# Performance work log

Hardware: AMD Instinct MI355X
Metric: run time of the kernel (lower is better)

The kernel has to match this reference:

```python
import jax, jax.numpy as jnp
import numpy as np

B, T, C = 4, 2048, 1024
WIN = 16


def setup_inputs() -> dict:
    key = jax.random.key(0)
    ks = jax.random.split(key, 5)
    s = 1.0 / np.sqrt(C)
    return {
        "x": jax.random.normal(ks[0], (B, T, C), dtype=jnp.float32),
        "Wq": jax.random.normal(ks[1], (C, C), dtype=jnp.float32) * s,
        "bq": jnp.zeros((C,), jnp.float32),
        "Wk": jax.random.normal(ks[2], (C, C), dtype=jnp.float32) * s,
        "bk": jnp.zeros((C,), jnp.float32),
        "Wv": jax.random.normal(ks[3], (C, C), dtype=jnp.float32) * s,
        "bv": jnp.zeros((C,), jnp.float32),
        "Wo": jax.random.normal(ks[4], (C, C), dtype=jnp.float32) * s,
        "bo": jnp.zeros((C,), jnp.float32),
        "window": WIN,
    }


def reference(x, Wq, bq, Wk, bk, Wv, bv, Wo, bo, window):
    Bn, Tn, Cn = x.shape
    half = window // 2
    W = 2 * half + 1  # keys per query (window [t-half, t+half])
    q = x @ Wq.T + bq
    k = x @ Wk.T + bk
    v = x @ Wv.T + bv
    offs = jnp.arange(-half, half + 1)              # [W]
    tpos = jnp.arange(Tn)                            # [T]
    idx = tpos[:, None] + offs[None, :]              # [T, W]
    valid = (idx >= 0) & (idx < Tn)                  # [T, W]
    idx_c = jnp.clip(idx, 0, Tn - 1)
    k_win = k[:, idx_c, :]                           # [B, T, W, C]
    v_win = v[:, idx_c, :]                           # [B, T, W, C]
    scale = 1.0 / jnp.sqrt(jnp.asarray(Cn, x.dtype))
    scores = jnp.einsum('btc,btwc->btw', q, k_win) * scale
    scores = jnp.where(valid[None, :, :], scores, jnp.finfo(x.dtype).min)
    attn = jax.nn.softmax(scores, axis=-1)           # [B, T, W]
    ctx = jnp.einsum('btw,btwc->btc', attn, v_win)   # [B, T, C]
    return ctx @ Wo.T + bo
```

## Files before the change

### kernel.cpp

```cpp
#include <hip/hip_runtime.h>
#include <cstdint>
#include <cstddef>

#define B_ 4
#define T_ 2048
#define C_ 1024
#define M_ (B_ * T_)
#define HALF_ 8
#define W_ 17
#define QKV_STRIDE 3072

typedef unsigned short u16;
typedef _Float16 half8 __attribute__((ext_vector_type(8)));
typedef _Float16 half2_t __attribute__((ext_vector_type(2)));
typedef float f32x16 __attribute__((ext_vector_type(16)));

__device__ __forceinline__ float dot16(half8 a, half8 b, float acc) {
#if __has_builtin(__builtin_amdgcn_fdot2)
    const half2_t* pa = (const half2_t*)&a;
    const half2_t* pb = (const half2_t*)&b;
#pragma unroll
    for (int e = 0; e < 4; ++e) acc = __builtin_amdgcn_fdot2(pa[e], pb[e], acc, false);
#else
#pragma unroll
    for (int e = 0; e < 8; ++e) acc += (float)a[e] * (float)b[e];
#endif
    return acc;
}

__device__ __forceinline__ ushort4 cvt4(float4 v) {
    ushort4 o;
    _Float16 a = (_Float16)v.x; o.x = __builtin_bit_cast(unsigned short, a);
    _Float16 b = (_Float16)v.y; o.y = __builtin_bit_cast(unsigned short, b);
    _Float16 c = (_Float16)v.z; o.z = __builtin_bit_cast(unsigned short, c);
    _Float16 d = (_Float16)v.w; o.w = __builtin_bit_cast(unsigned short, d);
    return o;
}


__global__ void prologue(const float* __restrict__ x,
                         const float* __restrict__ Wq, const float* __restrict__ Wk,
                         const float* __restrict__ Wv, const float* __restrict__ Wo,
                         const float* __restrict__ bq, const float* __restrict__ bk,
                         const float* __restrict__ bv,
                         u16* __restrict__ xf, u16* __restrict__ wfq,
                         u16* __restrict__ wfo, float* __restrict__ bcat) {
    const int blk = blockIdx.x;
    const int tid = threadIdx.x;
    if (blk < 4096) {
        const int wid  = blk * 4 + (tid >> 6);
        const int lane = tid & 63;
        const int mt = wid >> 6;
        const int ks = wid & 63;
        const int row = mt * 32 + (lane & 31);
        const int col = ks * 16 + (lane >> 5) * 8;
        const float4* s = (const float4*)(x + (size_t)row * C_ + col);
        ushort4* d = (ushort4*)(xf + (((size_t)mt * 64 + ks) * 64 + lane) * 8);
        d[0] = cvt4(s[0]);
        d[1] = cvt4(s[1]);
        return;
    }
    if (blk >= 6144) {
        int i = (blk - 6144) * 256 + tid;
        const float* src = (i < 1024) ? bq : (i < 2048) ? bk : bv;
        bcat[i] = src[i & 1023];
        return;
    }
    int c = (blk - 4096) * 256 + tid;
    const float* src;
    u16* dst;
    int cc;
    if (c < 393216) {
        int mat = c / 131072;
        src = (mat == 0) ? Wq : (mat == 1) ? Wk : Wv;
        dst = wfq;  cc = c;  c = c % 131072;
    } else {
        src = Wo;  dst = wfo;  cc = c - 393216;  c = cc;
    }
    const int nt_local = c >> 12;
    const int ks   = (c >> 6) & 63;
    const int lane = c & 63;
    const int row = nt_local * 32 + (lane & 31);
    const int col = ks * 16 + (lane >> 5) * 8;
    const float4* s = (const float4*)(src + (size_t)row * C_ + col);
    ushort4* d = (ushort4*)(dst + (size_t)cc * 8);
    d[0] = cvt4(s[0]);
    d[1] = cvt4(s[1]);
}

template <int OUT_F16>
__global__ __launch_bounds__(256) void gemm_frag(
    const u16* __restrict__ Afrag, const u16* __restrict__ Bfrag,
    const float* __restrict__ bias, void* __restrict__ Cout,
    int Ndim, int nks)
{
    const int tid  = threadIdx.x;
    const int lane = tid & 63;
    const int wave = tid >> 6;
    const int m0 = blockIdx.y * 128;
    const int wm = (wave >> 1) * 64;
    const int mt0 = blockIdx.y * 4 + (wave >> 1) * 2;
    const int wnt = blockIdx.x * 4 + (wave & 1) * 2;

    const u16* Af0 = Afrag + ((size_t)mt0 * nks) * 512 + lane * 8;
    const u16* Af1 = Af0 + (size_t)nks * 512;
    const u16* Bf0 = Bfrag + ((size_t)wnt * nks) * 512 + lane * 8;
    const u16* Bf1 = Bf0 + (size_t)nks * 512;

    f32x16 acc00, acc01, acc10, acc11;
#pragma unroll
    for (int r = 0; r < 16; ++r) { acc00[r] = 0.f; acc01[r] = 0.f; acc10[r] = 0.f; acc11[r] = 0.f; }

#pragma unroll 4
    for (int ks = 0; ks < nks; ++ks) {
        const size_t off = (size_t)ks * 512;
        half8 a0 = *(const half8*)(Af0 + off);
        half8 a1 = *(const half8*)(Af1 + off);
        half8 b0 = *(const half8*)(Bf0 + off);
        half8 b1 = *(const half8*)(Bf1 + off);
        acc00 = __builtin_amdgcn_mfma_f32_32x32x16_f16(a0, b0, acc00, 0, 0, 0);
        acc01 = __builtin_amdgcn_mfma_f32_32x32x16_f16(a0, b1, acc01, 0, 0, 0);
        acc10 = __builtin_amdgcn_mfma_f32_32x32x16_f16(a1, b0, acc10, 0, 0, 0);
        acc11 = __builtin_amdgcn_mfma_f32_32x32x16_f16(a1, b1, acc11, 0, 0, 0);
    }

    f32x16 accs[2][2] = {{acc00, acc01}, {acc10, acc11}};
#pragma unroll
    for (int i = 0; i < 2; ++i) {
#pragma unroll
        for (int j = 0; j < 2; ++j) {
            const int col = (wnt + j) * 32 + (lane & 31);
            const float bv = bias[col];
#pragma unroll
            for (int reg = 0; reg < 16; ++reg) {
                const int row = m0 + wm + i * 32 + (reg & 3) + 8 * (reg >> 2) + 4 * (lane >> 5);
                float val = accs[i][j][reg] + bv;
                if (OUT_F16) {
                    _Float16 h = (_Float16)val;
                    ((u16*)Cout)[(size_t)row * Ndim + col] = __builtin_bit_cast(unsigned short, h);
                } else {
                    ((float*)Cout)[(size_t)row * Ndim + col] = val;
                }
            }
        }
    }
}

__global__ __launch_bounds__(256) void attn_local(
    const u16* __restrict__ qkv, u16* __restrict__ ctxf)
{
    const int wid  = blockIdx.x * 4 + (threadIdx.x >> 6);
    const int lane = threadIdx.x & 63;
    const int b = wid >> 11;
    const int t = wid & (T_ - 1);
    const int base = b * T_;
    const size_t qrow = (size_t)(base + t) * QKV_STRIDE;
    const int c0 = lane * 8;

    half8 q0 = *(const half8*)(qkv + qrow + c0);
    half8 q1 = *(const half8*)(qkv + qrow + 512 + c0);

    float s[W_];
#pragma unroll
    for (int o = 0; o < W_; ++o) {
        int j = t - HALF_ + o;
        int jc = min(max(j, 0), T_ - 1);
        const size_t kb = (size_t)(base + jc) * QKV_STRIDE + 1024;
        half8 k0v = *(const half8*)(qkv + kb + c0);
        half8 k1v = *(const half8*)(qkv + kb + 512 + c0);
        float d = dot16(q1, k1v, dot16(q0, k0v, 0.f));
#pragma unroll
        for (int off = 32; off > 0; off >>= 1)
            d += __shfl_xor(d, off);
        s[o] = (j == jc) ? d * 0.03125f : -3.0e38f;
    }

    float mx = s[0];
#pragma unroll
    for (int o = 1; o < W_; ++o) mx = fmaxf(mx, s[o]);
    float den = 0.f;
#pragma unroll
    for (int o = 0; o < W_; ++o) den += __expf(s[o] - mx);
    const float inv = 1.f / den;

    float acc0[8], acc1[8];
#pragma unroll
    for (int e = 0; e < 8; ++e) { acc0[e] = 0.f; acc1[e] = 0.f; }
#pragma unroll
    for (int o = 0; o < W_; ++o) {
        int j = t - HALF_ + o;
        int jc = min(max(j, 0), T_ - 1);
        const float wt = __expf(s[o] - mx) * inv;
        const size_t vb_ = (size_t)(base + jc) * QKV_STRIDE + 2048;
        half8 v0 = *(const half8*)(qkv + vb_ + c0);
        half8 v1 = *(const half8*)(qkv + vb_ + 512 + c0);
#pragma unroll
        for (int e = 0; e < 8; ++e) {
            acc0[e] += wt * (float)v0[e];
            acc1[e] += wt * (float)v1[e];
        }
    }

    half8 o0, o1;
#pragma unroll
    for (int e = 0; e < 8; ++e) { o0[e] = (_Float16)acc0[e]; o1[e] = (_Float16)acc1[e]; }

    const int m = base + t;
    const int mt = m >> 5;
    const int rowin = (m & 31) + 32 * (lane & 1);
    const size_t ch0 = ((size_t)mt * 64 + (lane >> 1)) * 64 + rowin;
    const size_t ch1 = ((size_t)mt * 64 + 32 + (lane >> 1)) * 64 + rowin;
    *(half8*)(ctxf + ch0 * 8) = o0;
    *(half8*)(ctxf + ch1 * 8) = o1;
}

extern "C" void kernel_launch(void* const* d_in, const int* in_sizes, int n_in,
                              void* d_out, int out_size, void* d_ws, size_t ws_size,
                              hipStream_t stream) {
    const float* x  = (const float*)d_in[0];
    const float* Wq = (const float*)d_in[1];
    const float* bq = (const float*)d_in[2];
    const float* Wk = (const float*)d_in[3];
    const float* bk = (const float*)d_in[4];
    const float* Wv = (const float*)d_in[5];
    const float* bv = (const float*)d_in[6];
    const float* Wo = (const float*)d_in[7];
    const float* bo = (const float*)d_in[8];
    float* out = (float*)d_out;

    u16* xf   = (u16*)d_ws;
    u16* wfq  = xf   + (size_t)M_ * C_;
    u16* wfo  = wfq  + (size_t)3 * C_ * C_;
    u16* qkvh = wfo  + (size_t)C_ * C_;
    u16* ctxf = qkvh + (size_t)M_ * QKV_STRIDE;
    float* bcat = (float*)(ctxf + (size_t)M_ * C_);

    prologue<<<6156, 256, 0, stream>>>(x, Wq, Wk, Wv, Wo, bq, bk, bv,
                                       xf, wfq, wfo, bcat);

    dim3 gqkv(QKV_STRIDE / 128, M_ / 128);
    gemm_frag<1><<<gqkv, 256, 0, stream>>>(xf, wfq, bcat, qkvh, QKV_STRIDE, 64);

    attn_local<<<M_ / 4, 256, 0, stream>>>(qkvh, ctxf);

    dim3 go(C_ / 128, M_ / 128);
    gemm_frag<0><<<go, 256, 0, stream>>>(ctxf, wfo, bo, out, C_, 64);
}
```

Before: 228.0 us.

## Rewrite fragment GEMM with LDS triple-buffered async loads and 8-wave blocks

Replaces the direct-from-global fragment GEMM with a 512-thread, 256x128-tile kernel that stages A and B fragments into a three-slot LDS ring using global_load_lds. Each K step overlaps the prefetch of the tile two steps ahead with MFMA work, coordinated by barriers, wave priority raising and explicit vmcnt waits. Operands loaded into LDS are shared across waves, which cuts redundant global traffic. The cost is roughly 144KB of LDS per block, which limits occupancy, plus many barriers and fragile hand-placed waitcnt logic.

```diff
diff --git a/kernel.cpp b/kernel.cpp
--- a/kernel.cpp
+++ b/kernel.cpp
@@ -9,6 +9,8 @@
 #define HALF_ 8
 #define W_ 17
 #define QKV_STRIDE 3072
+#define NKS 64
+#define NT 16
 
 typedef unsigned short u16;
 typedef _Float16 half8 __attribute__((ext_vector_type(8)));
@@ -88,52 +90,147 @@
     d[1] = cvt4(s[1]);
 }
 
+
+#define AS1_ __attribute__((address_space(1)))
+#define AS3_ __attribute__((address_space(3)))
+
+__device__ __forceinline__ void gload16(const u16* g, u16* l) {
+    __builtin_amdgcn_global_load_lds((AS1_ void*)g, (AS3_ void*)l, 16, 0, 0);
+}
+
+#define MFMA_ __builtin_amdgcn_mfma_f32_32x32x16_f16
+
+#define GEMM_ITER(CB, NB, KT)                                                  \
+  {                                                                            \
+                                 \
+    half8 a00 = *(const half8*)((CB) + offA0);                                 \
+    half8 a01 = *(const half8*)((CB) + offA0 + 512);                           \
+    half8 a10 = *(const half8*)((CB) + offA1);                                 \
+    half8 a11 = *(const half8*)((CB) + offA1 + 512);                           \
+    half8 p00 = *(const half8*)((CB) + offB0);                                 \
+    half8 p01 = *(const half8*)((CB) + offB0 + 512);                           \
+    half8 p10 = *(const half8*)((CB) + offB1);                                 \
+    half8 p11 = *(const half8*)((CB) + offB1 + 512);                           \
+    if ((KT) + 2 < NT) {                                                       \
+      const size_t ko = (size_t)((KT) + 2) * 2048;                             \
+      gload16(gs0 + ko, (NB) + lo0);                                           \
+      gload16(gs1 + ko, (NB) + lo1);                                           \
+      gload16(gs2 + ko, (NB) + lo2);                                           \
+      gload16(gs3 + ko, (NB) + lo3);                                           \
+    }                                                                          \
+    asm volatile("s_barrier" ::: "memory");                                    \
+    __builtin_amdgcn_s_setprio(1);                                             \
+    acc00 = MFMA_(a00, p00, acc00, 0, 0, 0);                                   \
+    acc01 = MFMA_(a00, p10, acc01, 0, 0, 0);                                   \
+    acc10 = MFMA_(a10, p00, acc10, 0, 0, 0);                                   \
+    acc11 = MFMA_(a10, p10, acc11, 0, 0, 0);                                   \
+    acc00 = MFMA_(a01, p01, acc00, 0, 0, 0);                                   \
+    acc01 = MFMA_(a01, p11, acc01, 0, 0, 0);                                   \
+    acc10 = MFMA_(a11, p01, acc10, 0, 0, 0);                                   \
+    acc11 = MFMA_(a11, p11, acc11, 0, 0, 0);                                   \
+    __builtin_amdgcn_s_setprio(0);                                             \
+    asm volatile("s_barrier" ::: "memory");                                    \
+                                                \
+    a00 = *(const half8*)((CB) + offA0 + 1024);                                \
+    a01 = *(const half8*)((CB) + offA0 + 1536);                                \
+    a10 = *(const half8*)((CB) + offA1 + 1024);                                \
+    a11 = *(const half8*)((CB) + offA1 + 1536);                                \
+    p00 = *(const half8*)((CB) + offB0 + 1024);                                \
+    p01 = *(const half8*)((CB) + offB0 + 1536);                                \
+    p10 = *(const half8*)((CB) + offB1 + 1024);                                \
+    p11 = *(const half8*)((CB) + offB1 + 1536);                                \
+    if ((KT) + 2 < NT) {                                                       \
+      const size_t ko = (size_t)((KT) + 2) * 2048;                             \
+      gload16(gs4 + ko, (NB) + lo4);                                           \
+      gload16(gs5 + ko, (NB) + lo5);                                           \
+    }                                                                          \
+    asm volatile("s_barrier" ::: "memory");                                    \
+    __builtin_amdgcn_s_setprio(1);                                             \
+    acc00 = MFMA_(a00, p00, acc00, 0, 0, 0);                                   \
+    acc01 = MFMA_(a00, p10, acc01, 0, 0, 0);                                   \
+    acc10 = MFMA_(a10, p00, acc10, 0, 0, 0);                                   \
+    acc11 = MFMA_(a10, p10, acc11, 0, 0, 0);                                   \
+    acc00 = MFMA_(a01, p01, acc00, 0, 0, 0);                                   \
+    acc01 = MFMA_(a01, p11, acc01, 0, 0, 0);                                   \
+    acc10 = MFMA_(a11, p01, acc10, 0, 0, 0);                                   \
+    acc11 = MFMA_(a11, p11, acc11, 0, 0, 0);                                   \
+    __builtin_amdgcn_s_setprio(0);                                             \
+       \
+                              \
+    asm volatile("s_waitcnt lgkmcnt(0)" ::: "memory");                         \
+    if ((KT) == NT - 2) asm volatile("s_waitcnt vmcnt(0)" ::: "memory");       \
+    else                asm volatile("s_waitcnt vmcnt(6)" ::: "memory");       \
+    asm volatile("s_barrier" ::: "memory");                                    \
+  }
+
 template <int OUT_F16>
-__global__ __launch_bounds__(256) void gemm_frag(
+__global__ __launch_bounds__(512, 2) void gemm_8ph(
     const u16* __restrict__ Afrag, const u16* __restrict__ Bfrag,
-    const float* __restrict__ bias, void* __restrict__ Cout,
-    int Ndim, int nks)
+    const float* __restrict__ bias, void* __restrict__ Cout, int Ndim)
 {
+    __shared__ u16 lds[3][24576];
     const int tid  = threadIdx.x;
     const int lane = tid & 63;
     const int wave = tid >> 6;
-    const int m0 = blockIdx.y * 128;
-    const int wm = (wave >> 1) * 64;
-    const int mt0 = blockIdx.y * 4 + (wave >> 1) * 2;
-    const int wnt = blockIdx.x * 4 + (wave & 1) * 2;
-
-    const u16* Af0 = Afrag + ((size_t)mt0 * nks) * 512 + lane * 8;
-    const u16* Af1 = Af0 + (size_t)nks * 512;
-    const u16* Bf0 = Bfrag + ((size_t)wnt * nks) * 512 + lane * 8;
-    const u16* Bf1 = Bf0 + (size_t)nks * 512;
+    const int wm   = wave >> 1;
+    const int wn   = wave & 1;
+    const int bx = blockIdx.x, by = blockIdx.y;
+    const int la8 = lane * 8;
+
+    const int offA0 = wm * 4096 + la8;
+    const int offA1 = offA0 + 2048;
+    const int offB0 = 16384 + wn * 4096 + la8;
+    const int offB1 = offB0 + 2048;
+
+    const u16* gs0 = Afrag + ((size_t)(by*8 + ((wave+ 0)>>2))*64 + ((wave+ 0)&3))*512 + la8;
+    const u16* gs1 = Afrag + ((size_t)(by*8 + ((wave+ 8)>>2))*64 + ((wave+ 8)&3))*512 + la8;
+    const u16* gs2 = Afrag + ((size_t)(by*8 + ((wave+16)>>2))*64 + ((wave+16)&3))*512 + la8;
+    const u16* gs3 = Afrag + ((size_t)(by*8 + ((wave+24)>>2))*64 + ((wave+24)&3))*512 + la8;
+    const u16* gs4 = Bfrag + ((size_t)(bx*4 + ((wave+ 0)>>2))*64 + ((wave+ 0)&3))*512 + la8;
+    const u16* gs5 = Bfrag + ((size_t)(bx*4 + ((wave+ 8)>>2))*64 + ((wave+ 8)&3))*512 + la8;
+    const int lo0 = (wave +  0) * 512;
+    const int lo1 = (wave +  8) * 512;
+    const int lo2 = (wave + 16) * 512;
+    const int lo3 = (wave + 24) * 512;
+    const int lo4 = 16384 + (wave + 0) * 512;
+    const int lo5 = 16384 + (wave + 8) * 512;
+
+    u16* b0 = &lds[0][0];
+    u16* b1 = &lds[1][0];
+    u16* b2 = &lds[2][0];
+
+    gload16(gs0, b0 + lo0); gload16(gs1, b0 + lo1); gload16(gs2, b0 + lo2);
+    gload16(gs3, b0 + lo3); gload16(gs4, b0 + lo4); gload16(gs5, b0 + lo5);
+    gload16(gs0 + 2048, b1 + lo0); gload16(gs1 + 2048, b1 + lo1);
+    gload16(gs2 + 2048, b1 + lo2); gload16(gs3 + 2048, b1 + lo3);
+    gload16(gs4 + 2048, b1 + lo4); gload16(gs5 + 2048, b1 + lo5);
+    asm volatile("s_waitcnt vmcnt(6)" ::: "memory");
+    asm volatile("s_barrier" ::: "memory");
 
     f32x16 acc00, acc01, acc10, acc11;
 #pragma unroll
     for (int r = 0; r < 16; ++r) { acc00[r] = 0.f; acc01[r] = 0.f; acc10[r] = 0.f; acc11[r] = 0.f; }
 
-#pragma unroll 4
-    for (int ks = 0; ks < nks; ++ks) {
-        const size_t off = (size_t)ks * 512;
-        half8 a0 = *(const half8*)(Af0 + off);
-        half8 a1 = *(const half8*)(Af1 + off);
-        half8 b0 = *(const half8*)(Bf0 + off);
-        half8 b1 = *(const half8*)(Bf1 + off);
-        acc00 = __builtin_amdgcn_mfma_f32_32x32x16_f16(a0, b0, acc00, 0, 0, 0);
-        acc01 = __builtin_amdgcn_mfma_f32_32x32x16_f16(a0, b1, acc01, 0, 0, 0);
-        acc10 = __builtin_amdgcn_mfma_f32_32x32x16_f16(a1, b0, acc10, 0, 0, 0);
-        acc11 = __builtin_amdgcn_mfma_f32_32x32x16_f16(a1, b1, acc11, 0, 0, 0);
-    }
-
+#pragma unroll 1
+    for (int kt = 0; kt < NT - 1; kt += 3) {
+        GEMM_ITER(b0, b2, kt);
+        GEMM_ITER(b1, b0, kt + 1);
+        GEMM_ITER(b2, b1, kt + 2);
+    }
+    GEMM_ITER(b0, b2, NT - 1);
+
+    const int m0 = by * 256 + wm * 64;
+    const int n0 = bx * 128 + wn * 64;
     f32x16 accs[2][2] = {{acc00, acc01}, {acc10, acc11}};
 #pragma unroll
     for (int i = 0; i < 2; ++i) {
 #pragma unroll
         for (int j = 0; j < 2; ++j) {
-            const int col = (wnt + j) * 32 + (lane & 31);
+            const int col = n0 + j * 32 + (lane & 31);
             const float bv = bias[col];
 #pragma unroll
             for (int reg = 0; reg < 16; ++reg) {
-                const int row = m0 + wm + i * 32 + (reg & 3) + 8 * (reg >> 2) + 4 * (lane >> 5);
+                const int row = m0 + i * 32 + (reg & 3) + 8 * (reg >> 2) + 4 * (lane >> 5);
                 float val = accs[i][j][reg] + bv;
                 if (OUT_F16) {
                     _Float16 h = (_Float16)val;
@@ -238,11 +335,11 @@
     prologue<<<6156, 256, 0, stream>>>(x, Wq, Wk, Wv, Wo, bq, bk, bv,
                                        xf, wfq, wfo, bcat);
 
-    dim3 gqkv(QKV_STRIDE / 128, M_ / 128);
-    gemm_frag<1><<<gqkv, 256, 0, stream>>>(xf, wfq, bcat, qkvh, QKV_STRIDE, 64);
+    dim3 gqkv(QKV_STRIDE / 128, M_ / 256);
+    gemm_8ph<1><<<gqkv, 512, 0, stream>>>(xf, wfq, bcat, qkvh, QKV_STRIDE);
 
     attn_local<<<M_ / 4, 256, 0, stream>>>(qkvh, ctxf);
 
-    dim3 go(C_ / 128, M_ / 128);
-    gemm_frag<0><<<go, 256, 0, stream>>>(ctxf, wfo, bo, out, C_, 64);
-}
+    dim3 go(C_ / 128, M_ / 256);
+    gemm_8ph<0><<<go, 512, 0, stream>>>(ctxf, wfo, bo, out, C_);
+}
```

Measured after the change: 229.4 us. Within noise of the previous version (+0.6%).

## Pipeline GEMMs through LDS with async global loads and coalesce prologue conversion

Applied to the files above, without the earlier changes.

Replaces the register-direct fragment GEMM with a 256x128 block tile whose operands are staged through a triple-buffered LDS ring using global_load_lds. The loop hand-schedules waitcnt and barriers, raises wave priority around the MFMA bursts, and swizzles block order for L2 locality. The prologue now converts fp32 to fp16 through a swizzled shared-memory transpose so global reads and writes coalesce. The aim is to hide global memory latency and raise data reuse per block. It costs more LDS and registers and relies on fragile manual vmcnt accounting.

```diff
diff --git a/kernel.cpp b/kernel.cpp
--- a/kernel.cpp
+++ b/kernel.cpp
@@ -9,11 +9,13 @@
 #define HALF_ 8
 #define W_ 17
 #define QKV_STRIDE 3072
+#define NT 32
 
 typedef unsigned short u16;
 typedef _Float16 half8 __attribute__((ext_vector_type(8)));
 typedef _Float16 half2_t __attribute__((ext_vector_type(2)));
 typedef float f32x16 __attribute__((ext_vector_type(16)));
+typedef unsigned short ushort8v __attribute__((ext_vector_type(8)));
 
 __device__ __forceinline__ float dot16(half8 a, half8 b, float acc) {
 #if __has_builtin(__builtin_amdgcn_fdot2)
@@ -38,102 +40,189 @@
 }
 
 
-__global__ void prologue(const float* __restrict__ x,
-                         const float* __restrict__ Wq, const float* __restrict__ Wk,
-                         const float* __restrict__ Wv, const float* __restrict__ Wo,
-                         const float* __restrict__ bq, const float* __restrict__ bk,
-                         const float* __restrict__ bv,
-                         u16* __restrict__ xf, u16* __restrict__ wfq,
-                         u16* __restrict__ wfo, float* __restrict__ bcat) {
+__global__ void prologue2(const float* __restrict__ x,
+                          const float* __restrict__ Wq, const float* __restrict__ Wk,
+                          const float* __restrict__ Wv, const float* __restrict__ Wo,
+                          const float* __restrict__ bq, const float* __restrict__ bk,
+                          const float* __restrict__ bv,
+                          u16* __restrict__ xf, u16* __restrict__ wfq,
+                          u16* __restrict__ wfo, float* __restrict__ bcat) {
     const int blk = blockIdx.x;
     const int tid = threadIdx.x;
-    if (blk < 4096) {
-        const int wid  = blk * 4 + (tid >> 6);
-        const int lane = tid & 63;
-        const int mt = wid >> 6;
-        const int ks = wid & 63;
-        const int row = mt * 32 + (lane & 31);
-        const int col = ks * 16 + (lane >> 5) * 8;
-        const float4* s = (const float4*)(x + (size_t)row * C_ + col);
-        ushort4* d = (ushort4*)(xf + (((size_t)mt * 64 + ks) * 64 + lane) * 8);
-        d[0] = cvt4(s[0]);
-        d[1] = cvt4(s[1]);
-        return;
-    }
-    if (blk >= 6144) {
-        int i = (blk - 6144) * 256 + tid;
+    if (blk >= 3072) {
+        int i = (blk - 3072) * 256 + tid;
         const float* src = (i < 1024) ? bq : (i < 2048) ? bk : bv;
         bcat[i] = src[i & 1023];
         return;
     }
-    int c = (blk - 4096) * 256 + tid;
+    __shared__ ushort8v g16[512];
     const float* src;
     u16* dst;
-    int cc;
-    if (c < 393216) {
-        int mat = c / 131072;
-        src = (mat == 0) ? Wq : (mat == 1) ? Wk : Wv;
-        dst = wfq;  cc = c;  c = c % 131072;
+    size_t chunk_base;
+    int kg;
+    if (blk < 2048) {
+        const int mt = blk >> 3; kg = blk & 7;
+        src = x + (size_t)mt * 32 * C_;
+        dst = xf; chunk_base = (size_t)mt * 64;
     } else {
-        src = Wo;  dst = wfo;  cc = c - 393216;  c = cc;
-    }
-    const int nt_local = c >> 12;
-    const int ks   = (c >> 6) & 63;
-    const int lane = c & 63;
-    const int row = nt_local * 32 + (lane & 31);
-    const int col = ks * 16 + (lane >> 5) * 8;
-    const float4* s = (const float4*)(src + (size_t)row * C_ + col);
-    ushort4* d = (ushort4*)(dst + (size_t)cc * 8);
-    d[0] = cvt4(s[0]);
-    d[1] = cvt4(s[1]);
-}
+        const int w = blk - 2048;
+        const int mat = w >> 8, nt = (w >> 3) & 31; kg = w & 7;
+        src = ((mat == 0) ? Wq : (mat == 1) ? Wk : (mat == 2) ? Wv : Wo)
+              + (size_t)nt * 32 * C_;
+        if (mat < 3) { dst = wfq; chunk_base = (size_t)(mat * 32 + nt) * 64; }
+        else         { dst = wfo; chunk_base = (size_t)nt * 64; }
+    }
+    const int r = tid >> 3, gc = (tid & 7) * 2;
+    const float4* s4 = (const float4*)(src + (size_t)r * C_ + kg * 128 + (tid & 7) * 16);
+    float4 f0 = s4[0], f1 = s4[1], f2 = s4[2], f3 = s4[3];
+    ushort4 h0 = cvt4(f0), h1 = cvt4(f1), h2 = cvt4(f2), h3 = cvt4(f3);
+    ushort8v ga, gb;
+    ga[0]=h0.x; ga[1]=h0.y; ga[2]=h0.z; ga[3]=h0.w;
+    ga[4]=h1.x; ga[5]=h1.y; ga[6]=h1.z; ga[7]=h1.w;
+    gb[0]=h2.x; gb[1]=h2.y; gb[2]=h2.z; gb[3]=h2.w;
+    gb[4]=h3.x; gb[5]=h3.y; gb[6]=h3.z; gb[7]=h3.w;
+    g16[r * 16 + ((gc    ) ^ (r & 15))] = ga;
+    g16[r * 16 + ((gc + 1) ^ (r & 15))] = gb;
+    __syncthreads();
+    const int lane = tid & 63, rr = lane & 31, hi = lane >> 5;
+#pragma unroll
+    for (int r2 = 0; r2 < 2; ++r2) {
+        const int ksl = r2 * 4 + (tid >> 6);
+        const int g = ksl * 2 + hi;
+        ushort8v v = g16[rr * 16 + (g ^ (rr & 15))];
+        *(ushort8v*)(dst + ((chunk_base + kg * 8 + ksl) * 64 + lane) * 8) = v;
+    }
+}
+
+
+#define AS1_ __attribute__((address_space(1)))
+#define AS3_ __attribute__((address_space(3)))
+
+__device__ __forceinline__ void gload16(const u16* g, u16* l) {
+    __builtin_amdgcn_global_load_lds((AS1_ void*)g, (AS3_ void*)l, 16, 0, 0);
+}
+
+#define MFMA_ __builtin_amdgcn_mfma_f32_32x32x16_f16
+
+#define STAGE(NB, KT) { const size_t ko = (size_t)(KT) * 1024;            \
+    gload16(gA0 + ko, (NB) + lA0); gload16(gA1 + ko, (NB) + lA1);         \
+    gload16(gA2 + ko, (NB) + lA2); gload16(gA3 + ko, (NB) + lA3);         \
+    gload16(gB0 + ko, (NB) + lB0); gload16(gB1 + ko, (NB) + lB1); }
+
+#define TILE(CB, NB, KT, DOSTG, VW)                                        \
+  {                                                                        \
+    half8 a0 = *(const half8*)((CB) + oA);                                 \
+    half8 a1 = *(const half8*)((CB) + oA + 1024);                          \
+    half8 a2 = *(const half8*)((CB) + oA + 2048);                          \
+    half8 a3 = *(const half8*)((CB) + oA + 3072);                          \
+    half8 b0v = *(const half8*)((CB) + oB);                                \
+    half8 b1v = *(const half8*)((CB) + oB + 1024);                         \
+    if (DOSTG) STAGE(NB, (KT) + 2);                                        \
+    __builtin_amdgcn_s_setprio(1);                                         \
+    acc00 = MFMA_(a0, b0v, acc00, 0, 0, 0);                                \
+    acc01 = MFMA_(a0, b1v, acc01, 0, 0, 0);                                \
+    acc10 = MFMA_(a1, b0v, acc10, 0, 0, 0);                                \
+    acc11 = MFMA_(a1, b1v, acc11, 0, 0, 0);                                \
+    acc20 = MFMA_(a2, b0v, acc20, 0, 0, 0);                                \
+    acc21 = MFMA_(a2, b1v, acc21, 0, 0, 0);                                \
+    acc30 = MFMA_(a3, b0v, acc30, 0, 0, 0);                                \
+    acc31 = MFMA_(a3, b1v, acc31, 0, 0, 0);                                \
+    __builtin_amdgcn_s_setprio(0);                                         \
+    a0 = *(const half8*)((CB) + oA + 512);                                 \
+    a1 = *(const half8*)((CB) + oA + 1536);                                \
+    a2 = *(const half8*)((CB) + oA + 2560);                                \
+    a3 = *(const half8*)((CB) + oA + 3584);                                \
+    b0v = *(const half8*)((CB) + oB + 512);                                \
+    b1v = *(const half8*)((CB) + oB + 1536);                               \
+    __builtin_amdgcn_s_setprio(1);                                         \
+    acc00 = MFMA_(a0, b0v, acc00, 0, 0, 0);                                \
+    acc01 = MFMA_(a0, b1v, acc01, 0, 0, 0);                                \
+    acc10 = MFMA_(a1, b0v, acc10, 0, 0, 0);                                \
+    acc11 = MFMA_(a1, b1v, acc11, 0, 0, 0);                                \
+    acc20 = MFMA_(a2, b0v, acc20, 0, 0, 0);                                \
+    acc21 = MFMA_(a2, b1v, acc21, 0, 0, 0);                                \
+    acc30 = MFMA_(a3, b0v, acc30, 0, 0, 0);                                \
+    acc31 = MFMA_(a3, b1v, acc31, 0, 0, 0);                                \
+    __builtin_amdgcn_s_setprio(0);                                         \
+     \
+    if ((VW) == 6)      asm volatile("s_waitcnt vmcnt(6) lgkmcnt(0)" ::: "memory"); \
+    else if ((VW) == 0) asm volatile("s_waitcnt vmcnt(0) lgkmcnt(0)" ::: "memory"); \
+    else                asm volatile("s_waitcnt lgkmcnt(0)" ::: "memory"); \
+    asm volatile("s_barrier" ::: "memory");                                \
+  }
 
 template <int OUT_F16>
-__global__ __launch_bounds__(256) void gemm_frag(
+__global__ __launch_bounds__(256, 2) void gemm_p2(
     const u16* __restrict__ Afrag, const u16* __restrict__ Bfrag,
-    const float* __restrict__ bias, void* __restrict__ Cout,
-    int Ndim, int nks)
+    const float* __restrict__ bias, void* __restrict__ Cout, int Ndim)
 {
+    __shared__ u16 lds[3][12288];
     const int tid  = threadIdx.x;
     const int lane = tid & 63;
     const int wave = tid >> 6;
-    const int m0 = blockIdx.y * 128;
-    const int wm = (wave >> 1) * 64;
-    const int mt0 = blockIdx.y * 4 + (wave >> 1) * 2;
-    const int wnt = blockIdx.x * 4 + (wave & 1) * 2;
-
-    const u16* Af0 = Afrag + ((size_t)mt0 * nks) * 512 + lane * 8;
-    const u16* Af1 = Af0 + (size_t)nks * 512;
-    const u16* Bf0 = Bfrag + ((size_t)wnt * nks) * 512 + lane * 8;
-    const u16* Bf1 = Bf0 + (size_t)nks * 512;
-
-    f32x16 acc00, acc01, acc10, acc11;
-#pragma unroll
-    for (int r = 0; r < 16; ++r) { acc00[r] = 0.f; acc01[r] = 0.f; acc10[r] = 0.f; acc11[r] = 0.f; }
-
-#pragma unroll 4
-    for (int ks = 0; ks < nks; ++ks) {
-        const size_t off = (size_t)ks * 512;
-        half8 a0 = *(const half8*)(Af0 + off);
-        half8 a1 = *(const half8*)(Af1 + off);
-        half8 b0 = *(const half8*)(Bf0 + off);
-        half8 b1 = *(const half8*)(Bf1 + off);
-        acc00 = __builtin_amdgcn_mfma_f32_32x32x16_f16(a0, b0, acc00, 0, 0, 0);
-        acc01 = __builtin_amdgcn_mfma_f32_32x32x16_f16(a0, b1, acc01, 0, 0, 0);
-        acc10 = __builtin_amdgcn_mfma_f32_32x32x16_f16(a1, b0, acc10, 0, 0, 0);
-        acc11 = __builtin_amdgcn_mfma_f32_32x32x16_f16(a1, b1, acc11, 0, 0, 0);
-    }
-
-    f32x16 accs[2][2] = {{acc00, acc01}, {acc10, acc11}};
-#pragma unroll
-    for (int i = 0; i < 2; ++i) {
+    const int wm   = wave >> 1;
+    const int wn   = wave & 1;
+    const int la8  = lane * 8;
+
+    const int nb  = gridDim.x * gridDim.y;
+    int bid = blockIdx.y * gridDim.x + blockIdx.x;
+    bid = (bid & 7) * (nb >> 3) + (bid >> 3);
+    const int bx = bid % gridDim.x;
+    const int by = bid / gridDim.x;
+
+    const u16* gA0 = Afrag + ((size_t)(by*8 + ((wave    )>>1))*64 + ((wave    )&1))*512 + la8;
+    const u16* gA1 = Afrag + ((size_t)(by*8 + ((wave+ 4 )>>1))*64 + ((wave+ 4 )&1))*512 + la8;
+    const u16* gA2 = Afrag + ((size_t)(by*8 + ((wave+ 8 )>>1))*64 + ((wave+ 8 )&1))*512 + la8;
+    const u16* gA3 = Afrag + ((size_t)(by*8 + ((wave+12 )>>1))*64 + ((wave+12 )&1))*512 + la8;
+    const u16* gB0 = Bfrag + ((size_t)(bx*4 + ((wave    )>>1))*64 + ((wave    )&1))*512 + la8;
+    const u16* gB1 = Bfrag + ((size_t)(bx*4 + ((wave+ 4 )>>1))*64 + ((wave+ 4 )&1))*512 + la8;
+    const int lA0 = (wave     ) * 512;
+    const int lA1 = (wave +  4) * 512;
+    const int lA2 = (wave +  8) * 512;
+    const int lA3 = (wave + 12) * 512;
+    const int lB0 = 8192 + (wave    ) * 512;
+    const int lB1 = 8192 + (wave + 4) * 512;
+
+    const int oA = wm * 4096 + la8;
+    const int oB = 8192 + wn * 2048 + la8;
+
+    u16* b0 = &lds[0][0];
+    u16* b1 = &lds[1][0];
+    u16* b2 = &lds[2][0];
+
+    STAGE(b0, 0);
+    STAGE(b1, 1);
+    asm volatile("s_waitcnt vmcnt(6)" ::: "memory");
+    asm volatile("s_barrier" ::: "memory");
+
+    f32x16 acc00, acc01, acc10, acc11, acc20, acc21, acc30, acc31;
+#pragma unroll
+    for (int r = 0; r < 16; ++r) {
+        acc00[r] = 0.f; acc01[r] = 0.f; acc10[r] = 0.f; acc11[r] = 0.f;
+        acc20[r] = 0.f; acc21[r] = 0.f; acc30[r] = 0.f; acc31[r] = 0.f;
+    }
+
+#pragma unroll 1
+    for (int kt = 0; kt < NT - 2; kt += 3) {
+        TILE(b0, b2, kt,     1, 6);
+        TILE(b1, b0, kt + 1, 1, 6);
+        TILE(b2, b1, kt + 2, 1, 6);
+    }
+    TILE(b0, b2, NT - 2, 0, 0);
+    TILE(b1, b2, NT - 1, 0, -1);
+
+    const int m0 = by * 256 + wm * 128;
+    const int n0 = bx * 128 + wn * 64;
+    f32x16 accs[4][2] = {{acc00, acc01}, {acc10, acc11}, {acc20, acc21}, {acc30, acc31}};
+#pragma unroll
+    for (int i = 0; i < 4; ++i) {
 #pragma unroll
         for (int j = 0; j < 2; ++j) {
-            const int col = (wnt + j) * 32 + (lane & 31);
+            const int col = n0 + j * 32 + (lane & 31);
             const float bv = bias[col];
 #pragma unroll
             for (int reg = 0; reg < 16; ++reg) {
-                const int row = m0 + wm + i * 32 + (reg & 3) + 8 * (reg >> 2) + 4 * (lane >> 5);
+                const int row = m0 + i * 32 + (reg & 3) + 8 * (reg >> 2) + 4 * (lane >> 5);
                 float val = accs[i][j][reg] + bv;
                 if (OUT_F16) {
                     _Float16 h = (_Float16)val;
@@ -235,14 +324,14 @@
     u16* ctxf = qkvh + (size_t)M_ * QKV_STRIDE;
     float* bcat = (float*)(ctxf + (size_t)M_ * C_);
 
-    prologue<<<6156, 256, 0, stream>>>(x, Wq, Wk, Wv, Wo, bq, bk, bv,
-                                       xf, wfq, wfo, bcat);
-
-    dim3 gqkv(QKV_STRIDE / 128, M_ / 128);
-    gemm_frag<1><<<gqkv, 256, 0, stream>>>(xf, wfq, bcat, qkvh, QKV_STRIDE, 64);
+    prologue2<<<3084, 256, 0, stream>>>(x, Wq, Wk, Wv, Wo, bq, bk, bv,
+                                        xf, wfq, wfo, bcat);
+
+    dim3 gqkv(QKV_STRIDE / 128, M_ / 256);
+    gemm_p2<1><<<gqkv, 256, 0, stream>>>(xf, wfq, bcat, qkvh, QKV_STRIDE);
 
     attn_local<<<M_ / 4, 256, 0, stream>>>(qkvh, ctxf);
 
-    dim3 go(C_ / 128, M_ / 128);
-    gemm_frag<0><<<go, 256, 0, stream>>>(ctxf, wfo, bo, out, C_, 64);
-}
+    dim3 go(C_ / 128, M_ / 256);
+    gemm_p2<0><<<go, 256, 0, stream>>>(ctxf, wfo, bo, out, C_);
+}
```

Measured after the change: 212.2 us. -6.9%, faster.
